# Optimization experiments

Hardware: AMD Instinct MI355X
Metric: run time of the kernel (lower is better)

Reference implementation:

```python
import jax, jax.numpy as jnp
import numpy as np

# Per-feature MLP topology from NAM._get_topology: 1->32->64->128->64->32->16->1
DIMS = [1, 32, 64, 128, 64, 32, 16, 1]
N_LAYERS = len(DIMS) - 1  # 7 linear layers
BATCH, DIM = 2048, 256


def setup_inputs() -> dict:
    key = jax.random.key(0)
    inp = {"x": jax.random.normal(jax.random.fold_in(key, 0), (BATCH, DIM), dtype=jnp.float32)}
    # Batched parameters: stack the `dim` independent tiny MLPs along a leading axis.
    # torch.nn.Linear default init: U(-1/sqrt(fan_in), 1/sqrt(fan_in)) for W and b.
    for l in range(N_LAYERS):
        fi, fo = DIMS[l], DIMS[l + 1]
        kw, kb = jax.random.split(jax.random.fold_in(key, l + 1))
        bound = 1.0 / np.sqrt(fi)
        inp[f"W{l}"] = jax.random.uniform(kw, (DIM, fi, fo), jnp.float32, -bound, bound)
        inp[f"b{l}"] = jax.random.uniform(kb, (DIM, fo), jnp.float32, -bound, bound)
    return inp


def reference(x, W0, b0, W1, b1, W2, b2, W3, b3, W4, b4, W5, b5, W6, b6):
    Ws = [W0, W1, W2, W3, W4, W5, W6]
    bs = [b0, b1, b2, b3, b4, b5, b6]
    # h: [batch, dim, feat] — all `dim` tiny MLPs run as one batched GEMM per layer
    h = x[:, :, None]
    for l in range(N_LAYERS):
        h = jnp.einsum('bdi,dio->bdo', h, Ws[l]) + bs[l][None, :, :]
        if l < N_LAYERS - 1:
            h = jax.nn.relu(h)
    # funcs_sum = sum over features of each per-feature scalar output -> [batch, 1]
    return jnp.sum(h, axis=1)
```

## Files before the change

kernel.cpp:

```cpp
#include <hip/hip_runtime.h>

#define BATCH 2048
#define DIM   256
#define WAVES 8

typedef _Float16 half8 __attribute__((ext_vector_type(8)));
typedef _Float16 half4 __attribute__((ext_vector_type(4)));
typedef __attribute__((ext_vector_type(4))) float f32x4;

#define NTILES 41
#define TILE_HALVES 512

template <int FI, int FO, int LBASE, bool EXTRACT>
__device__ __forceinline__ void layer_mfma(
    const _Float16* __restrict__ packs,
    const float* __restrict__ bld,
    int m, int q, int lane, _Float16* __restrict__ bw,
    const half8 (*A)[4], half8 (*O)[4]) {
  constexpr int KT = FI / 32, NT = FO / 16;
#pragma unroll
  for (int nt = 0; nt < NT; ++nt) {
    const float bias = bld[nt * 16 + m];
    f32x4 acc[4];
#pragma unroll
    for (int rt = 0; rt < 4; ++rt) acc[rt] = {bias, bias, bias, bias};
#pragma unroll
    for (int kt = 0; kt < KT; ++kt) {
      const _Float16* tb = packs + (size_t)(LBASE + nt * KT + kt) * TILE_HALVES;
      const half8 Bh = *(const half8*)(tb + lane * 8);
#pragma unroll
      for (int rt = 0; rt < 4; ++rt)
        acc[rt] = __builtin_amdgcn_mfma_f32_16x16x32_f16(A[rt][kt], Bh, acc[rt], 0, 0, 0);
    }
    const int hcol = (nt & 1) * 16 + m;
#pragma unroll
    for (int rt = 0; rt < 4; ++rt)
#pragma unroll
      for (int r = 0; r < 4; ++r)
        bw[rt * 576 + (q * 4 + r) * 36 + hcol] =
            (_Float16)fmaxf(acc[rt][r], 0.0f);
    if (EXTRACT && (nt & 1)) {
      const int ktn = nt >> 1;
#pragma unroll
      for (int rt = 0; rt < 4; ++rt) {
        const _Float16* p = &bw[rt * 576 + m * 36 + q * 8];
        const half4 v0 = *(const half4*)p;
        const half4 v1 = *(const half4*)(p + 4);
        half8 o;
#pragma unroll
        for (int j = 0; j < 4; ++j) { o[j] = v0[j]; o[4 + j] = v1[j]; }
        O[rt][ktn] = o;
      }
    }
  }
}

__global__ __launch_bounds__(512, 2) void mlp_fused(
    const float* __restrict__ x,
    const float* __restrict__ W0, const float* __restrict__ b0,
    const float* __restrict__ W1, const float* __restrict__ b1,
    const float* __restrict__ W2, const float* __restrict__ b2,
    const float* __restrict__ W3, const float* __restrict__ b3,
    const float* __restrict__ W4, const float* __restrict__ b4,
    const float* __restrict__ W5, const float* __restrict__ b5,
    const float* __restrict__ W6, const float* __restrict__ b6,
    float* __restrict__ partial) {
  const int t = threadIdx.x;
  const int lane = t & 63;
  const int wave = t >> 6;
  const int m = lane & 15, q = lane >> 4;
  const int d = blockIdx.x;
  const int half = blockIdx.y;

  __shared__ __align__(16) _Float16 packs[NTILES * TILE_HALVES];
  __shared__ __align__(16) _Float16 act[WAVES][4 * 576];

  for (int job = t; job < NTILES * 64; job += 512) {
    const int tile = job >> 6, jl = job & 63;
    const int jm = jl & 15, jq = jl >> 4;
    const float* W; int FI, FO, lt;
    if (tile < 4)       { W = W1; FI = 32;  FO = 64;  lt = tile; }
    else if (tile < 20) { W = W2; FI = 64;  FO = 128; lt = tile - 4; }
    else if (tile < 36) { W = W3; FI = 128; FO = 64;  lt = tile - 20; }
    else if (tile < 40) { W = W4; FI = 64;  FO = 32;  lt = tile - 36; }
    else                { W = W5; FI = 32;  FO = 16;  lt = 0; }
    const int KT = FI >> 5;
    const int nt = lt / KT, kt = lt - nt * KT;
    const float* Wp = W + (size_t)d * FI * FO +
                      (size_t)(kt * 32 + jq * 8) * FO + nt * 16 + jm;
    half8 hi;
#pragma unroll
    for (int j = 0; j < 8; ++j) hi[j] = (_Float16)Wp[(size_t)j * FO];
    *(half8*)(packs + (size_t)tile * TILE_HALVES + jl * 8) = hi;
  }

  float w0r[8], b0r[8];
#pragma unroll
  for (int j = 0; j < 8; ++j) {
    w0r[j] = W0[d * 32 + q * 8 + j];
    b0r[j] = b0[d * 32 + q * 8 + j];
  }
  const float w6 = W6[d * 16 + m];
  const float bias6 = b6[d];

  __syncthreads();

  _Float16* bw = act[wave];
  half8 A0[4][4], A1[4][4];

  for (int it = 0; it < 2; ++it) {
    const int row0 = half * 1024 + it * 512 + wave * 64;

#pragma unroll
    for (int rt = 0; rt < 4; ++rt) {
      const float xv = x[(size_t)(row0 + rt * 16 + m) * DIM + d];
      half8 h;
#pragma unroll
      for (int j = 0; j < 8; ++j)
        h[j] = (_Float16)fmaxf(fmaf(xv, w0r[j], b0r[j]), 0.0f);
      A0[rt][0] = h;
    }

    layer_mfma<32, 64, 0, true>(packs, b1 + d * 64, m, q, lane, bw, A0, A1);
    layer_mfma<64, 128, 4, true>(packs, b2 + d * 128, m, q, lane, bw, A1, A0);
    layer_mfma<128, 64, 20, true>(packs, b3 + d * 64, m, q, lane, bw, A0, A1);
    layer_mfma<64, 32, 36, true>(packs, b4 + d * 32, m, q, lane, bw, A1, A0);
    layer_mfma<32, 16, 40, false>(packs, b5 + d * 16, m, q, lane, bw, A0, A1);

#pragma unroll
    for (int rt = 0; rt < 4; ++rt) {
#pragma unroll
      for (int r = 0; r < 4; ++r) {
        float v = (float)bw[rt * 576 + (q * 4 + r) * 36 + m] * w6;
        v += __shfl_xor(v, 1);
        v += __shfl_xor(v, 2);
        v += __shfl_xor(v, 4);
        v += __shfl_xor(v, 8);
        if (m == 0)
          partial[(size_t)d * BATCH + row0 + rt * 16 + q * 4 + r] = v + bias6;
      }
    }
  }
}

__global__ __launch_bounds__(256) void reduce_kernel(
    const float* __restrict__ partial, float* __restrict__ out) {
  const int b = blockIdx.x * blockDim.x + threadIdx.x;
  float s = 0.0f;
#pragma unroll 8
  for (int d = 0; d < DIM; ++d) s += partial[(size_t)d * BATCH + b];
  out[b] = s;
}

extern "C" void kernel_launch(void* const* d_in, const int* in_sizes, int n_in,
                              void* d_out, int out_size, void* d_ws, size_t ws_size,
                              hipStream_t stream) {
  const float* x = (const float*)d_in[0];
  const float* W[7];
  const float* B[7];
  for (int l = 0; l < 7; ++l) {
    W[l] = (const float*)d_in[1 + 2 * l];
    B[l] = (const float*)d_in[2 + 2 * l];
  }
  float* partial = (float*)d_ws;

  mlp_fused<<<dim3(DIM, 2), dim3(512), 0, stream>>>(
      x, W[0], B[0], W[1], B[1], W[2], B[2], W[3], B[3], W[4], B[4], W[5], B[5],
      W[6], B[6], partial);

  reduce_kernel<<<dim3(BATCH / 256), dim3(256), 0, stream>>>(partial,
                                                             (float*)d_out);
}
```

Before: 153.7 us.

## Compute transposed MFMA outputs so activations stay in registers without LDS round-trips

Swaps the MFMA operand order so the per-layer outputs land directly in the register layout the next layer needs as its input fragment. This removes the per-wave LDS scratch, the scatter stores and the gather reloads between layers. To make that work, the weight packing permutes the K index. Biases and the first and last layer parameters are staged once into shared memory and read as vectors, and row tiles per wave drop from 4 to 2 with twice as many iterations, which lowers register pressure but gives less MFMA work per weight fragment load.

```diff
diff --git a/kernel.cpp b/kernel.cpp
--- a/kernel.cpp
+++ b/kernel.cpp
@@ -2,55 +2,63 @@
 
 #define BATCH 2048
 #define DIM   256
-#define WAVES 8
+#define RT    2
 
 typedef _Float16 half8 __attribute__((ext_vector_type(8)));
-typedef _Float16 half4 __attribute__((ext_vector_type(4)));
 typedef __attribute__((ext_vector_type(4))) float f32x4;
 
 #define NTILES 41
 #define TILE_HALVES 512
 
-template <int FI, int FO, int LBASE, bool EXTRACT>
-__device__ __forceinline__ void layer_mfma(
-    const _Float16* __restrict__ packs,
-    const float* __restrict__ bld,
-    int m, int q, int lane, _Float16* __restrict__ bw,
-    const half8 (*A)[4], half8 (*O)[4]) {
-  constexpr int KT = FI / 32, NT = FO / 16;
+#define P_W0 0
+#define P_B0 32
+#define P_W6 64
+#define P_B1 80
+#define P_B2 144
+#define P_B3 272
+#define P_B4 336
+#define P_B5 368
+#define P_B6 384
+#define P_TOT 385
+
+template <int FI, int FO, int LBASE, int PBIAS>
+__device__ __forceinline__ void layer(
+    const _Float16* __restrict__ packs, const float* __restrict__ pl,
+    int lane, int q, const half8 (*__restrict__ in)[4],
+    half8 (*__restrict__ out)[4]) {
+  constexpr int KT = FI / 32, NTP = FO / 32;
 #pragma unroll
-  for (int nt = 0; nt < NT; ++nt) {
-    const float bias = bld[nt * 16 + m];
-    f32x4 acc[4];
+  for (int ntp = 0; ntp < NTP; ++ntp) {
+    f32x4 acc[2][RT];
 #pragma unroll
-    for (int rt = 0; rt < 4; ++rt) acc[rt] = {bias, bias, bias, bias};
+    for (int h = 0; h < 2; ++h) {
+      const int mt = ntp * 2 + h;
+      const f32x4 bias = *(const f32x4*)(pl + PBIAS + mt * 16 + (q << 2));
+      const _Float16* tb =
+          packs + (size_t)(LBASE + mt * KT) * TILE_HALVES + lane * 8;
+      half8 wf = *(const half8*)tb;
 #pragma unroll
-    for (int kt = 0; kt < KT; ++kt) {
-      const _Float16* tb = packs + (size_t)(LBASE + nt * KT + kt) * TILE_HALVES;
-      const half8 Bh = *(const half8*)(tb + lane * 8);
+      for (int rt = 0; rt < RT; ++rt)
+        acc[h][rt] = __builtin_amdgcn_mfma_f32_16x16x32_f16(
+            wf, in[rt][0], bias, 0, 0, 0);
 #pragma unroll
-      for (int rt = 0; rt < 4; ++rt)
-        acc[rt] = __builtin_amdgcn_mfma_f32_16x16x32_f16(A[rt][kt], Bh, acc[rt], 0, 0, 0);
+      for (int kt = 1; kt < KT; ++kt) {
+        wf = *(const half8*)(tb + kt * TILE_HALVES);
+#pragma unroll
+        for (int rt = 0; rt < RT; ++rt)
+          acc[h][rt] = __builtin_amdgcn_mfma_f32_16x16x32_f16(
+              wf, in[rt][kt], acc[h][rt], 0, 0, 0);
+      }
     }
-    const int hcol = (nt & 1) * 16 + m;
 #pragma unroll
-    for (int rt = 0; rt < 4; ++rt)
+    for (int rt = 0; rt < RT; ++rt) {
+      half8 o;
 #pragma unroll
-      for (int r = 0; r < 4; ++r)
-        bw[rt * 576 + (q * 4 + r) * 36 + hcol] =
-            (_Float16)fmaxf(acc[rt][r], 0.0f);
-    if (EXTRACT && (nt & 1)) {
-      const int ktn = nt >> 1;
-#pragma unroll
-      for (int rt = 0; rt < 4; ++rt) {
-        const _Float16* p = &bw[rt * 576 + m * 36 + q * 8];
-        const half4 v0 = *(const half4*)p;
-        const half4 v1 = *(const half4*)(p + 4);
-        half8 o;
-#pragma unroll
-        for (int j = 0; j < 4; ++j) { o[j] = v0[j]; o[4 + j] = v1[j]; }
-        O[rt][ktn] = o;
+      for (int j = 0; j < 4; ++j) {
+        o[j]     = (_Float16)fmaxf(acc[0][rt][j], 0.0f);
+        o[4 + j] = (_Float16)fmaxf(acc[1][rt][j], 0.0f);
       }
+      out[rt][ntp] = o;
     }
   }
 }
@@ -70,10 +78,10 @@
   const int wave = t >> 6;
   const int m = lane & 15, q = lane >> 4;
   const int d = blockIdx.x;
-  const int half = blockIdx.y;
+  const int halfb = blockIdx.y;
 
   __shared__ __align__(16) _Float16 packs[NTILES * TILE_HALVES];
-  __shared__ __align__(16) _Float16 act[WAVES][4 * 576];
+  __shared__ __align__(16) float pl[P_TOT];
 
   for (int job = t; job < NTILES * 64; job += 512) {
     const int tile = job >> 6, jl = job & 63;
@@ -85,60 +93,76 @@
     else if (tile < 40) { W = W4; FI = 64;  FO = 32;  lt = tile - 36; }
     else                { W = W5; FI = 32;  FO = 16;  lt = 0; }
     const int KT = FI >> 5;
-    const int nt = lt / KT, kt = lt - nt * KT;
-    const float* Wp = W + (size_t)d * FI * FO +
-                      (size_t)(kt * 32 + jq * 8) * FO + nt * 16 + jm;
+    const int mt = lt / KT, kt = lt - mt * KT;
+    const float* Wp = W + (size_t)d * FI * FO + (size_t)kt * 32 * FO +
+                      mt * 16 + jm;
     half8 hi;
 #pragma unroll
-    for (int j = 0; j < 8; ++j) hi[j] = (_Float16)Wp[(size_t)j * FO];
+    for (int j = 0; j < 8; ++j) {
+      const int fi = 16 * (j >> 2) + 4 * jq + (j & 3);
+      hi[j] = (_Float16)Wp[(size_t)fi * FO];
+    }
     *(half8*)(packs + (size_t)tile * TILE_HALVES + jl * 8) = hi;
   }
-
-  float w0r[8], b0r[8];
-#pragma unroll
-  for (int j = 0; j < 8; ++j) {
-    w0r[j] = W0[d * 32 + q * 8 + j];
-    b0r[j] = b0[d * 32 + q * 8 + j];
+  for (int i = t; i < P_TOT; i += 512) {
+    float v;
+    if (i < 32)       v = W0[d * 32 + i];
+    else if (i < 64)  v = b0[d * 32 + i - 32];
+    else if (i < 80)  v = W6[d * 16 + i - 64];
+    else if (i < 144) v = b1[d * 64 + i - 80];
+    else if (i < 272) v = b2[d * 128 + i - 144];
+    else if (i < 336) v = b3[d * 64 + i - 272];
+    else if (i < 368) v = b4[d * 32 + i - 336];
+    else if (i < 384) v = b5[d * 16 + i - 368];
+    else              v = b6[d];
+    pl[i] = v;
   }
-  const float w6 = W6[d * 16 + m];
-  const float bias6 = b6[d];
 
   __syncthreads();
 
-  _Float16* bw = act[wave];
-  half8 A0[4][4], A1[4][4];
+  const f32x4 w0a = *(const f32x4*)(pl + P_W0 + 4 * q);
+  const f32x4 w0b = *(const f32x4*)(pl + P_W0 + 16 + 4 * q);
+  const f32x4 b0a = *(const f32x4*)(pl + P_B0 + 4 * q);
+  const f32x4 b0b = *(const f32x4*)(pl + P_B0 + 16 + 4 * q);
+  const f32x4 w6v = *(const f32x4*)(pl + P_W6 + 4 * q);
+  const float bias6 = pl[P_B6];
 
-  for (int it = 0; it < 2; ++it) {
-    const int row0 = half * 1024 + it * 512 + wave * 64;
+  half8 fr0[RT][4], fr1[RT][4];
+
+  for (int it = 0; it < 4; ++it) {
+    const int row0 = halfb * 1024 + it * 256 + wave * 32;
 
 #pragma unroll
-    for (int rt = 0; rt < 4; ++rt) {
+    for (int rt = 0; rt < RT; ++rt) {
       const float xv = x[(size_t)(row0 + rt * 16 + m) * DIM + d];
       half8 h;
 #pragma unroll
-      for (int j = 0; j < 8; ++j)
-        h[j] = (_Float16)fmaxf(fmaf(xv, w0r[j], b0r[j]), 0.0f);
-      A0[rt][0] = h;
+      for (int j = 0; j < 4; ++j) {
+        h[j]     = (_Float16)fmaxf(fmaf(xv, w0a[j], b0a[j]), 0.0f);
+        h[4 + j] = (_Float16)fmaxf(fmaf(xv, w0b[j], b0b[j]), 0.0f);
+      }
+      fr0[rt][0] = h;
     }
 
-    layer_mfma<32, 64, 0, true>(packs, b1 + d * 64, m, q, lane, bw, A0, A1);
-    layer_mfma<64, 128, 4, true>(packs, b2 + d * 128, m, q, lane, bw, A1, A0);
-    layer_mfma<128, 64, 20, true>(packs, b3 + d * 64, m, q, lane, bw, A0, A1);
-    layer_mfma<64, 32, 36, true>(packs, b4 + d * 32, m, q, lane, bw, A1, A0);
-    layer_mfma<32, 16, 40, false>(packs, b5 + d * 16, m, q, lane, bw, A0, A1);
+    layer<32, 64, 0, P_B1>(packs, pl, lane, q, fr0, fr1);
+    layer<64, 128, 4, P_B2>(packs, pl, lane, q, fr1, fr0);
+    layer<128, 64, 20, P_B3>(packs, pl, lane, q, fr0, fr1);
+    layer<64, 32, 36, P_B4>(packs, pl, lane, q, fr1, fr0);
 
+    const f32x4 bias5 = *(const f32x4*)(pl + P_B5 + 4 * q);
+    const half8 wf5 =
+        *(const half8*)(packs + (size_t)40 * TILE_HALVES + lane * 8);
 #pragma unroll
-    for (int rt = 0; rt < 4; ++rt) {
+    for (int rt = 0; rt < RT; ++rt) {
+      const f32x4 a5 = __builtin_amdgcn_mfma_f32_16x16x32_f16(
+          wf5, fr0[rt][0], bias5, 0, 0, 0);
+      float v = 0.0f;
 #pragma unroll
-      for (int r = 0; r < 4; ++r) {
-        float v = (float)bw[rt * 576 + (q * 4 + r) * 36 + m] * w6;
-        v += __shfl_xor(v, 1);
-        v += __shfl_xor(v, 2);
-        v += __shfl_xor(v, 4);
-        v += __shfl_xor(v, 8);
-        if (m == 0)
-          partial[(size_t)d * BATCH + row0 + rt * 16 + q * 4 + r] = v + bias6;
-      }
+      for (int r = 0; r < 4; ++r) v += fmaxf(a5[r], 0.0f) * w6v[r];
+      v += __shfl_xor(v, 16);
+      v += __shfl_xor(v, 32);
+      if (q == 0)
+        partial[(size_t)d * BATCH + row0 + rt * 16 + m] = v + bias6;
     }
   }
 }
```

After: 190.5 us. +23.9%, slower.
